# Kernel optimization log

Measured on AMD Instinct MI355X. Metric: run time of the kernel, lower is better.

## Reference

```python
import jax, jax.numpy as jnp
import numpy as np

B, N, C_IN = 32, 1024, 128
F0, F1, F2 = 64, 64, 64
OUT = 10
RATIOS = (0.8, 0.8)
EPS = 1e-5


def setup_inputs() -> dict:
    key = jax.random.key(0)
    ks = jax.random.split(key, 16)
    N_nodes = jax.random.randint(ks[0], (B,), N // 2, N + 1)
    mask = (jnp.arange(N)[None, :] < N_nodes[:, None]).astype(jnp.float32)
    x = jax.random.normal(ks[1], (B, N, C_IN), dtype=jnp.float32)
    # sparse-ish symmetric binary adjacency restricted to valid nodes
    A = (jax.random.uniform(ks[2], (B, N, N)) < 0.02).astype(jnp.float32)
    A = jnp.maximum(A, jnp.swapaxes(A, 1, 2))
    A = A * mask[:, :, None] * mask[:, None, :]
    def lin(k, fi, fo):
        b = 1.0 / np.sqrt(fi)
        kw, kb = jax.random.split(k)
        return (jax.random.uniform(kw, (fi, fo), minval=-b, maxval=b),
                jax.random.uniform(kb, (fo,), minval=-b, maxval=b))
    W0, b0 = lin(ks[3], C_IN, F0)
    W1, b1 = lin(ks[4], F0, F1)
    W2, b2 = lin(ks[5], F1, F2)
    bp0 = 1.0 / np.sqrt(F0)
    p0 = jax.random.uniform(ks[6], (F0, 1), minval=-bp0, maxval=bp0)
    bp1 = 1.0 / np.sqrt(F1)
    p1 = jax.random.uniform(ks[7], (F1, 1), minval=-bp1, maxval=bp1)
    Wfc, bfc = lin(ks[8], F2, OUT)
    return {"x": x, "A": A, "mask": mask, "N_nodes": N_nodes,
            "W0": W0, "b0": b0, "W1": W1, "b1": b1, "W2": W2, "b2": b2,
            "p0": p0, "p1": p1, "Wfc": Wfc, "bfc": bfc}


def _gconv(x, A, W, b):
    # Kipf-Welling normalized Laplacian conv, batched dense
    n = A.shape[1]
    A_hat = A + jnp.eye(n, dtype=A.dtype)[None]
    D = (jnp.sum(A_hat, axis=1) + EPS) ** -0.5  # [B,N]
    L = D[:, :, None] * A_hat * D[:, None, :]
    h = jnp.einsum('bnm,bmc->bnc', L, x) @ W + b
    return jax.nn.relu(h)


def _pool(x, A, mask, N_nodes, p, ratio):
    Bc, Nc, C = x.shape
    y = (x.reshape(Bc * Nc, C) @ p).reshape(Bc, Nc)
    y = y / jnp.sqrt(jnp.sum(p ** 2))
    N_remove = (N_nodes.astype(jnp.float32) * (1.0 - ratio)).astype(N_nodes.dtype)
    # remove the N_remove lowest-scoring valid nodes per graph
    y_eff = jnp.where(mask > 0, y, jnp.inf)
    ranks = jnp.argsort(jnp.argsort(y_eff, axis=1), axis=1)  # ascending rank
    new_mask = mask * (ranks >= N_remove[:, None]).astype(mask.dtype)
    x = x * jnp.tanh(y)[:, :, None] * new_mask[:, :, None]
    A = new_mask[:, :, None] * A * new_mask[:, None, :]
    return x, A, new_mask, N_nodes - N_remove


def reference(x, A, mask, N_nodes, W0, b0, W1, b1, W2, b2, p0, p1, Wfc, bfc):
    x = _gconv(x, A, W0, b0)
    x, A, mask, N_nodes = _pool(x, A, mask, N_nodes, p0, RATIOS[0])
    x = _gconv(x, A, W1, b1)
    x, A, mask, N_nodes = _pool(x, A, mask, N_nodes, p1, RATIOS[1])
    x = _gconv(x, A, W2, b2)
    x = jnp.max(x, axis=1)  # global max pool over nodes [B,F2]
    return x @ Wfc + bfc
```

## Files before the change

kernel.cpp:

```cpp
#include <hip/hip_runtime.h>
#include <cstdint>
#include <cstddef>

#define BB 32
#define NN 1024
#define CIN 128
#define FF 64
#define NOUT 10
#define CAP 128
#define EPSV 1e-5f

__global__ __launch_bounds__(256) void k_front(const float* __restrict__ A,
                                               const float* __restrict__ x,
                                               const float* __restrict__ W0,
                                               const int* __restrict__ Nn,
                                               const float* __restrict__ b2f,
                                               float* __restrict__ gmax,
                                               unsigned short* __restrict__ adj,
                                               int* __restrict__ cnt,
                                               float* __restrict__ c1,
                                               float* __restrict__ c2,
                                               float* __restrict__ T) {
    __shared__ __align__(16) float Wl[64 * 64];
    int tid = threadIdx.x;
    int wave = tid >> 6, lane = tid & 63;
    if (blockIdx.x >= 10240) {
        for (int i = tid; i < BB * 64; i += 256)
            gmax[i] = fmaxf(b2f[i & 63], 0.f);
        return;
    }
    if (blockIdx.x >= 8192) {
        int gid = blockIdx.x - 8192;
        int b = gid & 31;
        int cch = gid >> 5;
        if (cch * 16 >= Nn[b]) return;
        int row0 = (b << 10) + cch * 16;
        int rsub = lane >> 4, f0 = (lane & 15) * 4;
        int r = row0 + wave * 4 + rsub;
        const float4* xr = (const float4*)(x + (size_t)r * CIN);
        float4 acc = {0.f, 0.f, 0.f, 0.f};
#pragma unroll
        for (int kc = 0; kc < 2; ++kc) {
            if (kc) __syncthreads();
            for (int t = tid; t < 64 * 16; t += 256)
                ((float4*)Wl)[t] = ((const float4*)W0)[kc * 1024 + t];
            __syncthreads();
#pragma unroll 4
            for (int k4 = 0; k4 < 16; ++k4) {
                float4 xv = xr[kc * 16 + k4];
                float4 w0 = *(const float4*)&Wl[(k4 * 4 + 0) * 64 + f0];
                float4 w1 = *(const float4*)&Wl[(k4 * 4 + 1) * 64 + f0];
                float4 w2 = *(const float4*)&Wl[(k4 * 4 + 2) * 64 + f0];
                float4 w3 = *(const float4*)&Wl[(k4 * 4 + 3) * 64 + f0];
                acc.x += xv.x * w0.x; acc.y += xv.x * w0.y; acc.z += xv.x * w0.z; acc.w += xv.x * w0.w;
                acc.x += xv.y * w1.x; acc.y += xv.y * w1.y; acc.z += xv.y * w1.z; acc.w += xv.y * w1.w;
                acc.x += xv.z * w2.x; acc.y += xv.z * w2.y; acc.z += xv.z * w2.z; acc.w += xv.z * w2.w;
                acc.x += xv.w * w3.x; acc.y += xv.w * w3.y; acc.z += xv.w * w3.z; acc.w += xv.w * w3.w;
            }
        }
        *(float4*)&T[(size_t)r * 64 + f0] = acc;
    } else {
        int r = blockIdx.x * 4 + wave;
        int b = r >> 10;
        int Nb = Nn[b];
        int rl = r & 1023;
        if (rl >= Nb) {
            if (lane == 0) {
                cnt[r] = 0;
                float D = 1.0f / sqrtf(1.0f + EPSV);
                c1[r] = D;
                c2[r] = D * D;
            }
            return;
        }
        unsigned short* adjs = ((unsigned short*)Wl) + wave * CAP;
        const float4* Arow = (const float4*)(A + (size_t)r * NN);
        int nch = (Nb + 255) >> 8;
        float4 z4 = {0.f, 0.f, 0.f, 0.f};
        float4 v0 = Arow[lane];
        float4 v1 = Arow[64 + lane];
        float4 v2 = (nch > 2) ? Arow[128 + lane] : z4;
        float4 v3 = (nch > 3) ? Arow[192 + lane] : z4;
        int c = 0;
        unsigned long long lt = (lane == 0) ? 0ULL : ((1ULL << lane) - 1ULL);
        float4 vv[4] = {v0, v1, v2, v3};
#pragma unroll
        for (int it = 0; it < 4; ++it) {
            float4 v = vv[it];
            int j0 = it * 256 + lane * 4;
            unsigned long long m0 = __ballot(v.x != 0.f);
            unsigned long long m1 = __ballot(v.y != 0.f);
            unsigned long long m2 = __ballot(v.z != 0.f);
            unsigned long long m3 = __ballot(v.w != 0.f);
            int before = __popcll(m0 & lt) + __popcll(m1 & lt) +
                         __popcll(m2 & lt) + __popcll(m3 & lt);
            int p = c + before;
            if (v.x != 0.f) { if (p < CAP) adjs[p] = (unsigned short)(j0 + 0); ++p; }
            if (v.y != 0.f) { if (p < CAP) adjs[p] = (unsigned short)(j0 + 1); ++p; }
            if (v.z != 0.f) { if (p < CAP) adjs[p] = (unsigned short)(j0 + 2); ++p; }
            if (v.w != 0.f) { if (p < CAP) adjs[p] = (unsigned short)(j0 + 3); ++p; }
            c += __popcll(m0) + __popcll(m1) + __popcll(m2) + __popcll(m3);
        }
        int cc = (c > CAP) ? CAP : c;
        uint32_t* dst = (uint32_t*)(adj + (size_t)r * CAP);
        if (lane * 2 < cc) dst[lane] = ((const uint32_t*)adjs)[lane];
        if (lane == 0) {
            cnt[r] = cc;
            float D = 1.0f / sqrtf((float)c + 1.0f + EPSV);
            c1[r] = D;
            c2[r] = D * D;
        }
    }
}

__global__ __launch_bounds__(256) void k_spmm1(const unsigned short* __restrict__ adj,
                                               const int* __restrict__ cnt,
                                               const float* __restrict__ c1,
                                               const float* __restrict__ c2,
                                               const float* __restrict__ T,
                                               const float* __restrict__ bias,
                                               const float* __restrict__ p,
                                               float* __restrict__ y,
                                               const float* __restrict__ Wn,
                                               float* __restrict__ Tout,
                                               const int* __restrict__ Nn) {
    __shared__ __align__(16) float c1s[NN];
    int b   = blockIdx.x & 31;
    int cch = blockIdx.x >> 5;
    int Nb = Nn[b];
    if (cch * 16 >= Nb) return;
    int tid = threadIdx.x;
    int n4 = (Nb + 3) >> 2;
    if (tid < n4) ((float4*)c1s)[tid] = ((const float4*)(c1 + (b << 10)))[tid];
    __syncthreads();
    int wave = tid >> 6, lane = tid & 63;
    int r0 = (b << 10) + cch * 16 + wave * 4;
    const float* Tb = T + ((size_t)(b << 10) << 6);
    float bv = bias[lane];
    float pv = p[lane];
    float pp = pv * pv;
    for (int s = 32; s; s >>= 1) pp += __shfl_xor(pp, s, 64);
    float ppinv = 1.0f / sqrtf(pp);
#pragma unroll
    for (int rr = 0; rr < 4; ++rr) {
        int r = r0 + rr;
        int rl = r & 1023;
        if (rl >= Nb) break;
        const unsigned short* arow = adj + (size_t)r * CAP;
        int n = cnt[r];
        float acc0 = 0.f, acc1 = 0.f, acc2 = 0.f, acc3 = 0.f;
        int t = 0;
        for (; t + 4 <= n; t += 4) {
            ushort4 j4 = *(const ushort4*)(arow + t);
            acc0 += c1s[j4.x] * Tb[((int)j4.x << 6) + lane];
            acc1 += c1s[j4.y] * Tb[((int)j4.y << 6) + lane];
            acc2 += c1s[j4.z] * Tb[((int)j4.z << 6) + lane];
            acc3 += c1s[j4.w] * Tb[((int)j4.w << 6) + lane];
        }
        for (; t < n; ++t) {
            int j = arow[t];
            acc0 += c1s[j] * Tb[(j << 6) + lane];
        }
        float acc = (acc0 + acc1) + (acc2 + acc3);
        float o = c1s[rl] * acc + c2[r] * T[((size_t)r << 6) + lane] + bv;
        o = fmaxf(o, 0.f);
        {
            float a = o * pv;
            for (int s = 32; s; s >>= 1) a += __shfl_xor(a, s, 64);
            if (lane == 0) y[r] = a * ppinv;
        }
        {
            float tac = 0.f;
#pragma unroll 16
            for (int k = 0; k < 64; ++k)
                tac = fmaf(__shfl(o, k, 64), Wn[(k << 6) + lane], tac);
            Tout[((size_t)r << 6) + lane] = tac;
        }
    }
}

__global__ __launch_bounds__(256) void k_rankdeg(const float* __restrict__ y,
                                                 const float* __restrict__ maskSrc,
                                                 const int* __restrict__ nsrc,
                                                 const int* __restrict__ Nn,
                                                 const unsigned short* __restrict__ adj,
                                                 const int* __restrict__ cnt,
                                                 float* __restrict__ nmOut,
                                                 int* __restrict__ ncur,
                                                 float* __restrict__ csrcO,
                                                 float* __restrict__ scsO) {
    __shared__ __align__(16) float yv[NN];
    __shared__ __align__(16) unsigned long long kv[NN];
    __shared__ float nml[NN];
    int b = blockIdx.x;
    int tid = threadIdx.x;
    const float INF = __builtin_inff();
    int Nb = Nn[b];
    {
        float4 v;
        if (tid * 4 < Nb) {
            v = ((const float4*)(y + (b << 10)))[tid];
            float4 m = ((const float4*)(maskSrc + (b << 10)))[tid];
            v.x = (m.x > 0.f) ? v.x : INF;
            v.y = (m.y > 0.f) ? v.y : INF;
            v.z = (m.z > 0.f) ? v.z : INF;
            v.w = (m.w > 0.f) ? v.w : INF;
        } else {
            v.x = INF; v.y = INF; v.z = INF; v.w = INF;
        }
        ((float4*)yv)[tid] = v;
    }
    int n = nsrc[b];
    const float RM = (float)(1.0 - 0.8);
    int nrem = (int)((float)n * RM);
    if (tid == 0) ncur[b] = n - nrem;
    __syncthreads();
#pragma unroll
    for (int t = 0; t < 4; ++t) {
        int i = tid + (t << 8);
        unsigned int u = __float_as_uint(yv[i]);
        u ^= (unsigned int)((int)u >> 31) | 0x80000000u;
        kv[i] = ((unsigned long long)u << 10) | (unsigned int)i;
    }
    __syncthreads();
    unsigned long long k0 = kv[tid], k1 = kv[tid + 256],
                       k2 = kv[tid + 512], k3 = kv[tid + 768];
    int r0 = 0, r1 = 0, r2 = 0, r3 = 0;
    int nkc = (Nb + 1) >> 1;
#pragma unroll 4
    for (int c = 0; c < nkc; ++c) {
        ulonglong2 a = ((const ulonglong2*)kv)[c];
        r0 += (a.x < k0) + (a.y < k0);
        r1 += (a.x < k1) + (a.y < k1);
        r2 += (a.x < k2) + (a.y < k2);
        r3 += (a.x < k3) + (a.y < k3);
    }
    int rk[4] = {r0, r1, r2, r3};
#pragma unroll
    for (int t = 0; t < 4; ++t) {
        int i = tid + (t << 8);
        float nmv = (yv[i] < INF && rk[t] >= nrem) ? 1.f : 0.f;
        nml[i] = nmv;
        nmOut[(b << 10) + i] = nmv;
    }
    __syncthreads();
#pragma unroll
    for (int t = 0; t < 4; ++t) {
        int i = tid + (t << 8);
        if (i < Nb) {
            int gr = (b << 10) + i;
            float m = nml[i];
            int nn = cnt[gr];
            const unsigned short* ar = adj + (size_t)gr * CAP;
            float s = 0.f;
            int tt = 0;
            for (; tt + 4 <= nn; tt += 4) {
                ushort4 j4 = *(const ushort4*)(ar + tt);
                s += nml[j4.x] + nml[j4.y] + nml[j4.z] + nml[j4.w];
            }
            for (; tt < nn; ++tt) s += nml[ar[tt]];
            float D = 1.0f / sqrtf(m * s + 1.0f + EPSV);
            csrcO[gr] = m * D;
            scsO[gr] = tanhf(yv[i]) * m;
        }
    }
}

__global__ __launch_bounds__(256) void k_spmm23(const unsigned short* __restrict__ adj,
                                                const int* __restrict__ cnt,
                                                const float* __restrict__ csrc,
                                                const float* __restrict__ scs,
                                                const float* __restrict__ Tin,
                                                const float* __restrict__ bias,
                                                const float* __restrict__ p,
                                                float* __restrict__ y,
                                                const float* __restrict__ Wn,
                                                float* __restrict__ Tout,
                                                float* __restrict__ gmax,
                                                const int* __restrict__ Nn) {
    __shared__ __align__(16) float csrcs[NN];
    __shared__ __align__(16) float scss[NN];
    __shared__ float red[4][64];
    int b   = blockIdx.x & 31;
    int cch = blockIdx.x >> 5;
    int Nb = Nn[b];
    if (cch * 16 >= Nb) return;
    int tid = threadIdx.x;
    int n4 = (Nb + 3) >> 2;
    if (tid < n4) {
        ((float4*)csrcs)[tid] = ((const float4*)(csrc + (b << 10)))[tid];
        ((float4*)scss)[tid]  = ((const float4*)(scs  + (b << 10)))[tid];
    }
    __syncthreads();
    int wave = tid >> 6, lane = tid & 63;
    int r0 = (b << 10) + cch * 16 + wave * 4;
    const float* Tb = Tin + ((size_t)(b << 10) << 6);
    float bv = bias[lane];
    float pv = 0.f, ppinv = 0.f;
    if (p != nullptr) {
        pv = p[lane];
        float pp = pv * pv;
        for (int s = 32; s; s >>= 1) pp += __shfl_xor(pp, s, 64);
        ppinv = 1.0f / sqrtf(pp);
    }
    float vmax = 0.f;
#pragma unroll
    for (int rr = 0; rr < 4; ++rr) {
        int r = r0 + rr;
        int rl = r & 1023;
        if (rl >= Nb) break;
        const unsigned short* arow = adj + (size_t)r * CAP;
        int n = cnt[r];
        float acc0 = 0.f, acc1 = 0.f, acc2 = 0.f, acc3 = 0.f;
        int t = 0;
        for (; t + 4 <= n; t += 4) {
            ushort4 j4 = *(const ushort4*)(arow + t);
            acc0 += csrcs[j4.x] * (scss[j4.x] * Tb[((int)j4.x << 6) + lane]);
            acc1 += csrcs[j4.y] * (scss[j4.y] * Tb[((int)j4.y << 6) + lane]);
            acc2 += csrcs[j4.z] * (scss[j4.z] * Tb[((int)j4.z << 6) + lane]);
            acc3 += csrcs[j4.w] * (scss[j4.w] * Tb[((int)j4.w << 6) + lane]);
        }
        for (; t < n; ++t) {
            int j = arow[t];
            acc0 += csrcs[j] * (scss[j] * Tb[(j << 6) + lane]);
        }
        float acc = (acc0 + acc1) + (acc2 + acc3);
        float cd = csrcs[rl];
        float selfv = scss[rl] * Tin[((size_t)r << 6) + lane];
        float o = cd * acc + (cd * cd) * selfv + bv;
        o = fmaxf(o, 0.f);
        if (p != nullptr) {
            float a = o * pv;
            for (int s = 32; s; s >>= 1) a += __shfl_xor(a, s, 64);
            if (lane == 0) y[r] = a * ppinv;
        }
        if (Wn != nullptr) {
            float tac = 0.f;
#pragma unroll 16
            for (int k = 0; k < 64; ++k)
                tac = fmaf(__shfl(o, k, 64), Wn[(k << 6) + lane], tac);
            Tout[((size_t)r << 6) + lane] = tac;
        }
        vmax = fmaxf(vmax, o);
    }
    if (gmax != nullptr) {
        red[wave][lane] = vmax;
        __syncthreads();
        if (wave == 0) {
            float m = fmaxf(fmaxf(red[0][lane], red[1][lane]),
                            fmaxf(red[2][lane], red[3][lane]));
            atomicMax((int*)&gmax[(b << 6) + lane], __float_as_int(m));
        }
    }
}

__global__ __launch_bounds__(64) void k_fc(const float* __restrict__ gmax,
                                           const float* __restrict__ Wfc,
                                           const float* __restrict__ bfc,
                                           float* __restrict__ out) {
    __shared__ float gl[64];
    int b = blockIdx.x, lane = threadIdx.x;
    gl[lane] = gmax[(b << 6) + lane];
    __syncthreads();
    if (lane < NOUT) {
        float acc = bfc[lane];
        for (int k = 0; k < 64; ++k) acc += gl[k] * Wfc[k * NOUT + lane];
        out[b * NOUT + lane] = acc;
    }
}

extern "C" void kernel_launch(void* const* d_in, const int* in_sizes, int n_in,
                              void* d_out, int out_size, void* d_ws, size_t ws_size,
                              hipStream_t stream) {
    const float* x    = (const float*)d_in[0];
    const float* A    = (const float*)d_in[1];
    const float* mask = (const float*)d_in[2];
    const int*   Nn   = (const int*)d_in[3];
    const float* W0   = (const float*)d_in[4];
    const float* b0   = (const float*)d_in[5];
    const float* W1   = (const float*)d_in[6];
    const float* b1   = (const float*)d_in[7];
    const float* W2   = (const float*)d_in[8];
    const float* b2   = (const float*)d_in[9];
    const float* p0   = (const float*)d_in[10];
    const float* p1   = (const float*)d_in[11];
    const float* Wfc  = (const float*)d_in[12];
    const float* bfc  = (const float*)d_in[13];
    float* out = (float*)d_out;

    char* ws = (char*)d_ws;
    size_t off = 0;
    auto alloc = [&](size_t bytes) -> void* {
        void* p = ws + off;
        off = (off + bytes + 255) & ~(size_t)255;
        return p;
    };
    unsigned short* adj = (unsigned short*)alloc((size_t)BB * NN * CAP * 2);
    int*   cnt  = (int*)  alloc((size_t)BB * NN * 4);
    float* X    = (float*)alloc((size_t)BB * NN * 64 * 4);
    float* T    = (float*)alloc((size_t)BB * NN * 64 * 4);
    float* c1   = (float*)alloc((size_t)BB * NN * 4);
    float* c2   = (float*)alloc((size_t)BB * NN * 4);
    float* y    = (float*)alloc((size_t)BB * NN * 4);
    float* nm0  = (float*)alloc((size_t)BB * NN * 4);
    float* nm1  = (float*)alloc((size_t)BB * NN * 4);
    int*   nc0  = (int*)  alloc((size_t)BB * 4);
    int*   nc1  = (int*)  alloc((size_t)BB * 4);
    float* gmax = (float*)alloc((size_t)BB * 64 * 4);

    k_front<<<8192 + 2048 + 1, 256, 0, stream>>>(A, x, W0, Nn, b2, gmax,
                                                 adj, cnt, c1, c2, T);
    k_spmm1<<<2048, 256, 0, stream>>>(adj, cnt, c1, c2, T, b0, p0, y, W1, X, Nn);
    k_rankdeg<<<BB, 256, 0, stream>>>(y, mask, Nn, Nn, adj, cnt, nm0, nc0, c1, c2);
    k_spmm23<<<2048, 256, 0, stream>>>(adj, cnt, c1, c2, X, b1, p1, y, W2, T,
                                       nullptr, Nn);
    k_rankdeg<<<BB, 256, 0, stream>>>(y, nm0, nc0, Nn, adj, cnt, nm1, nc1, c1, c2);
    k_spmm23<<<2048, 256, 0, stream>>>(adj, cnt, c1, c2, T, b2, nullptr, nullptr,
                                       nullptr, nullptr, gmax, Nn);
    k_fc<<<BB, 64, 0, stream>>>(gmax, Wfc, bfc, out);
}
```

Before: 409.4 us.

## Aggregate-then-transform in sparse convs, split rank kernel, nontemporal input loads

The layer-2 and layer-3 graph convs now aggregate neighbours first, then apply the weight matrix through an LDS-staged 4-wide matmul, replacing the per-row shuffle-based transform. Rows removed by pooling are skipped. The rank/degree kernel is spread over 16 blocks per graph and uses a wave-parallel neighbour-mask sum, which raises parallelism beyond 32 blocks. Each sub-block still recomputes the full sort, so that work is duplicated. The large one-shot reads of A and x use nontemporal loads to reduce cache pollution.

```diff
diff --git a/kernel.cpp b/kernel.cpp
--- a/kernel.cpp
+++ b/kernel.cpp
@@ -9,6 +9,12 @@
 #define NOUT 10
 #define CAP 128
 #define EPSV 1e-5f
+
+typedef float vf4 __attribute__((ext_vector_type(4)));
+__device__ __forceinline__ float4 ldnt(const float4* p) {
+    vf4 v = __builtin_nontemporal_load((const vf4*)p);
+    return make_float4(v.x, v.y, v.z, v.w);
+}
 
 __global__ __launch_bounds__(256) void k_front(const float* __restrict__ A,
                                                const float* __restrict__ x,
@@ -47,7 +53,7 @@
             __syncthreads();
 #pragma unroll 4
             for (int k4 = 0; k4 < 16; ++k4) {
-                float4 xv = xr[kc * 16 + k4];
+                float4 xv = ldnt(xr + kc * 16 + k4);
                 float4 w0 = *(const float4*)&Wl[(k4 * 4 + 0) * 64 + f0];
                 float4 w1 = *(const float4*)&Wl[(k4 * 4 + 1) * 64 + f0];
                 float4 w2 = *(const float4*)&Wl[(k4 * 4 + 2) * 64 + f0];
@@ -77,10 +83,10 @@
         const float4* Arow = (const float4*)(A + (size_t)r * NN);
         int nch = (Nb + 255) >> 8;
         float4 z4 = {0.f, 0.f, 0.f, 0.f};
-        float4 v0 = Arow[lane];
-        float4 v1 = Arow[64 + lane];
-        float4 v2 = (nch > 2) ? Arow[128 + lane] : z4;
-        float4 v3 = (nch > 3) ? Arow[192 + lane] : z4;
+        float4 v0 = ldnt(Arow + lane);
+        float4 v1 = ldnt(Arow + 64 + lane);
+        float4 v2 = (nch > 2) ? ldnt(Arow + 128 + lane) : z4;
+        float4 v3 = (nch > 3) ? ldnt(Arow + 192 + lane) : z4;
         int c = 0;
         unsigned long long lt = (lane == 0) ? 0ULL : ((1ULL << lane) - 1ULL);
         float4 vv[4] = {v0, v1, v2, v3};
@@ -113,17 +119,16 @@
     }
 }
 
-__global__ __launch_bounds__(256) void k_spmm1(const unsigned short* __restrict__ adj,
-                                               const int* __restrict__ cnt,
-                                               const float* __restrict__ c1,
-                                               const float* __restrict__ c2,
-                                               const float* __restrict__ T,
-                                               const float* __restrict__ bias,
-                                               const float* __restrict__ p,
-                                               float* __restrict__ y,
-                                               const float* __restrict__ Wn,
-                                               float* __restrict__ Tout,
-                                               const int* __restrict__ Nn) {
+__global__ __launch_bounds__(256) void k_spmm(const unsigned short* __restrict__ adj,
+                                              const int* __restrict__ cnt,
+                                              const float* __restrict__ c1,
+                                              const float* __restrict__ c2,
+                                              const float* __restrict__ T,
+                                              const float* __restrict__ bias,
+                                              float* __restrict__ X,
+                                              const float* __restrict__ p,
+                                              float* __restrict__ y,
+                                              const int* __restrict__ Nn) {
     __shared__ __align__(16) float c1s[NN];
     int b   = blockIdx.x & 31;
     int cch = blockIdx.x >> 5;
@@ -164,18 +169,10 @@
         float acc = (acc0 + acc1) + (acc2 + acc3);
         float o = c1s[rl] * acc + c2[r] * T[((size_t)r << 6) + lane] + bv;
         o = fmaxf(o, 0.f);
-        {
-            float a = o * pv;
-            for (int s = 32; s; s >>= 1) a += __shfl_xor(a, s, 64);
-            if (lane == 0) y[r] = a * ppinv;
-        }
-        {
-            float tac = 0.f;
-#pragma unroll 16
-            for (int k = 0; k < 64; ++k)
-                tac = fmaf(__shfl(o, k, 64), Wn[(k << 6) + lane], tac);
-            Tout[((size_t)r << 6) + lane] = tac;
-        }
+        X[((size_t)r << 6) + lane] = o;
+        float a = o * pv;
+        for (int s = 32; s; s >>= 1) a += __shfl_xor(a, s, 64);
+        if (lane == 0) y[r] = a * ppinv;
     }
 }
 
@@ -187,15 +184,18 @@
                                                  const int* __restrict__ cnt,
                                                  float* __restrict__ nmOut,
                                                  int* __restrict__ ncur,
-                                                 float* __restrict__ csrcO,
-                                                 float* __restrict__ scsO) {
+                                                 float* __restrict__ cg,
+                                                 float* __restrict__ c1o,
+                                                 float* __restrict__ cso) {
     __shared__ __align__(16) float yv[NN];
     __shared__ __align__(16) unsigned long long kv[NN];
     __shared__ float nml[NN];
-    int b = blockIdx.x;
+    int b = blockIdx.x >> 4;
+    int sub = blockIdx.x & 15;
     int tid = threadIdx.x;
     const float INF = __builtin_inff();
     int Nb = Nn[b];
+    if ((sub << 6) >= Nb) return;
     {
         float4 v;
         if (tid * 4 < Nb) {
@@ -213,7 +213,7 @@
     int n = nsrc[b];
     const float RM = (float)(1.0 - 0.8);
     int nrem = (int)((float)n * RM);
-    if (tid == 0) ncur[b] = n - nrem;
+    if (sub == 0 && tid == 0) ncur[b] = n - nrem;
     __syncthreads();
 #pragma unroll
     for (int t = 0; t < 4; ++t) {
@@ -239,117 +239,147 @@
 #pragma unroll
     for (int t = 0; t < 4; ++t) {
         int i = tid + (t << 8);
-        float nmv = (yv[i] < INF && rk[t] >= nrem) ? 1.f : 0.f;
-        nml[i] = nmv;
-        nmOut[(b << 10) + i] = nmv;
-    }
-    __syncthreads();
-#pragma unroll
-    for (int t = 0; t < 4; ++t) {
-        int i = tid + (t << 8);
-        if (i < Nb) {
-            int gr = (b << 10) + i;
-            float m = nml[i];
+        nml[i] = (yv[i] < INF && rk[t] >= nrem) ? 1.f : 0.f;
+    }
+    __syncthreads();
+    int wave = tid >> 6, lane = tid & 63;
+    for (int rd = 0; rd < 16; ++rd) {
+        int i = (sub << 6) + (rd << 2) + wave;
+        int gr = (b << 10) + i;
+        if (i >= Nb) {
+            if (lane == 0) nmOut[gr] = 0.f;
+            continue;
+        }
+        float m = nml[i];
+        float s = 0.f;
+        if (m != 0.f) {
             int nn = cnt[gr];
             const unsigned short* ar = adj + (size_t)gr * CAP;
-            float s = 0.f;
-            int tt = 0;
-            for (; tt + 4 <= nn; tt += 4) {
-                ushort4 j4 = *(const ushort4*)(ar + tt);
-                s += nml[j4.x] + nml[j4.y] + nml[j4.z] + nml[j4.w];
-            }
-            for (; tt < nn; ++tt) s += nml[ar[tt]];
+            if (lane < nn)      s  = nml[ar[lane]];
+            if (lane + 64 < nn) s += nml[ar[lane + 64]];
+            for (int sh = 32; sh; sh >>= 1) s += __shfl_xor(s, sh, 64);
+        }
+        if (lane == 0) {
+            nmOut[gr] = m;
             float D = 1.0f / sqrtf(m * s + 1.0f + EPSV);
-            csrcO[gr] = m * D;
-            scsO[gr] = tanhf(yv[i]) * m;
-        }
-    }
-}
-
-__global__ __launch_bounds__(256) void k_spmm23(const unsigned short* __restrict__ adj,
-                                                const int* __restrict__ cnt,
-                                                const float* __restrict__ csrc,
-                                                const float* __restrict__ scs,
-                                                const float* __restrict__ Tin,
-                                                const float* __restrict__ bias,
-                                                const float* __restrict__ p,
-                                                float* __restrict__ y,
-                                                const float* __restrict__ Wn,
-                                                float* __restrict__ Tout,
-                                                float* __restrict__ gmax,
-                                                const int* __restrict__ Nn) {
-    __shared__ __align__(16) float csrcs[NN];
-    __shared__ __align__(16) float scss[NN];
-    __shared__ float red[4][64];
+            float th = tanhf(yv[i]);
+            cg[gr]  = (m * D) * th;
+            c1o[gr] = m * D;
+            cso[gr] = m * (D * D) * th;
+        }
+    }
+}
+
+__global__ __launch_bounds__(256) void k_spmmW(const unsigned short* __restrict__ adj,
+                                               const int* __restrict__ cnt,
+                                               const float* __restrict__ cg,
+                                               const float* __restrict__ c1,
+                                               const float* __restrict__ cs,
+                                               const float* __restrict__ Xin,
+                                               const float* __restrict__ W,
+                                               const float* __restrict__ bias,
+                                               const float* __restrict__ p,
+                                               float* __restrict__ y,
+                                               float* __restrict__ Xout,
+                                               float* __restrict__ gmax,
+                                               const int* __restrict__ Nn) {
+    __shared__ __align__(16) float Wl[64 * 64];
+    __shared__ __align__(16) float cgs[NN];
+    __shared__ __align__(16) float aggl[4][4][68];
+    __shared__ float4 red4[4][16];
     int b   = blockIdx.x & 31;
     int cch = blockIdx.x >> 5;
     int Nb = Nn[b];
     if (cch * 16 >= Nb) return;
     int tid = threadIdx.x;
+    for (int t = tid; t < 64 * 16; t += 256)
+        ((float4*)Wl)[t] = ((const float4*)W)[t];
     int n4 = (Nb + 3) >> 2;
-    if (tid < n4) {
-        ((float4*)csrcs)[tid] = ((const float4*)(csrc + (b << 10)))[tid];
-        ((float4*)scss)[tid]  = ((const float4*)(scs  + (b << 10)))[tid];
-    }
+    if (tid < n4) ((float4*)cgs)[tid] = ((const float4*)(cg + (b << 10)))[tid];
     __syncthreads();
     int wave = tid >> 6, lane = tid & 63;
     int r0 = (b << 10) + cch * 16 + wave * 4;
-    const float* Tb = Tin + ((size_t)(b << 10) << 6);
-    float bv = bias[lane];
-    float pv = 0.f, ppinv = 0.f;
-    if (p != nullptr) {
-        pv = p[lane];
-        float pp = pv * pv;
-        for (int s = 32; s; s >>= 1) pp += __shfl_xor(pp, s, 64);
-        ppinv = 1.0f / sqrtf(pp);
-    }
-    float vmax = 0.f;
+    const float* Xb = Xin + ((size_t)(b << 10) << 6);
+    int umask = 0;
 #pragma unroll
     for (int rr = 0; rr < 4; ++rr) {
         int r = r0 + rr;
         int rl = r & 1023;
-        if (rl >= Nb) break;
-        const unsigned short* arow = adj + (size_t)r * CAP;
-        int n = cnt[r];
-        float acc0 = 0.f, acc1 = 0.f, acc2 = 0.f, acc3 = 0.f;
-        int t = 0;
-        for (; t + 4 <= n; t += 4) {
-            ushort4 j4 = *(const ushort4*)(arow + t);
-            acc0 += csrcs[j4.x] * (scss[j4.x] * Tb[((int)j4.x << 6) + lane]);
-            acc1 += csrcs[j4.y] * (scss[j4.y] * Tb[((int)j4.y << 6) + lane]);
-            acc2 += csrcs[j4.z] * (scss[j4.z] * Tb[((int)j4.z << 6) + lane]);
-            acc3 += csrcs[j4.w] * (scss[j4.w] * Tb[((int)j4.w << 6) + lane]);
-        }
-        for (; t < n; ++t) {
-            int j = arow[t];
-            acc0 += csrcs[j] * (scss[j] * Tb[(j << 6) + lane]);
-        }
-        float acc = (acc0 + acc1) + (acc2 + acc3);
-        float cd = csrcs[rl];
-        float selfv = scss[rl] * Tin[((size_t)r << 6) + lane];
-        float o = cd * acc + (cd * cd) * selfv + bv;
-        o = fmaxf(o, 0.f);
-        if (p != nullptr) {
-            float a = o * pv;
-            for (int s = 32; s; s >>= 1) a += __shfl_xor(a, s, 64);
-            if (lane == 0) y[r] = a * ppinv;
-        }
-        if (Wn != nullptr) {
-            float tac = 0.f;
+        float aggv = 0.f;
+        if (rl < Nb) {
+            float c1r = c1[r];
+            if (c1r != 0.f) {
+                umask |= 1 << rr;
+                const unsigned short* arow = adj + (size_t)r * CAP;
+                int n = cnt[r];
+                float acc0 = 0.f, acc1 = 0.f, acc2 = 0.f, acc3 = 0.f;
+                int t = 0;
+                for (; t + 4 <= n; t += 4) {
+                    ushort4 j4 = *(const ushort4*)(arow + t);
+                    acc0 += cgs[j4.x] * Xb[((int)j4.x << 6) + lane];
+                    acc1 += cgs[j4.y] * Xb[((int)j4.y << 6) + lane];
+                    acc2 += cgs[j4.z] * Xb[((int)j4.z << 6) + lane];
+                    acc3 += cgs[j4.w] * Xb[((int)j4.w << 6) + lane];
+                }
+                for (; t < n; ++t) {
+                    int j = arow[t];
+                    acc0 += cgs[j] * Xb[(j << 6) + lane];
+                }
+                float acc = (acc0 + acc1) + (acc2 + acc3);
+                aggv = c1r * acc + cs[r] * Xin[((size_t)r << 6) + lane];
+            }
+        }
+        aggl[wave][rr][lane] = aggv;
+    }
+    int rsub = lane >> 4, f0 = (lane & 15) * 4;
+    float4 o4 = *(const float4*)&bias[f0];
 #pragma unroll 16
-            for (int k = 0; k < 64; ++k)
-                tac = fmaf(__shfl(o, k, 64), Wn[(k << 6) + lane], tac);
-            Tout[((size_t)r << 6) + lane] = tac;
-        }
-        vmax = fmaxf(vmax, o);
+    for (int k = 0; k < 64; ++k) {
+        float a = aggl[wave][rsub][k];
+        float4 w = *(const float4*)&Wl[(k << 6) + f0];
+        o4.x = fmaf(a, w.x, o4.x); o4.y = fmaf(a, w.y, o4.y);
+        o4.z = fmaf(a, w.z, o4.z); o4.w = fmaf(a, w.w, o4.w);
+    }
+    o4.x = fmaxf(o4.x, 0.f); o4.y = fmaxf(o4.y, 0.f);
+    o4.z = fmaxf(o4.z, 0.f); o4.w = fmaxf(o4.w, 0.f);
+    bool live = (umask >> rsub) & 1;
+    int rOut = r0 + rsub;
+    if (Xout != nullptr && live)
+        *(float4*)&Xout[((size_t)rOut << 6) + f0] = o4;
+    if (p != nullptr) {
+        float4 p4 = *(const float4*)&p[f0];
+        float pp = p4.x * p4.x + p4.y * p4.y + p4.z * p4.z + p4.w * p4.w;
+        for (int s = 8; s; s >>= 1) pp += __shfl_xor(pp, s, 64);
+        float ppinv = 1.0f / sqrtf(pp);
+        float a = o4.x * p4.x + o4.y * p4.y + o4.z * p4.z + o4.w * p4.w;
+        for (int s = 8; s; s >>= 1) a += __shfl_xor(a, s, 64);
+        if ((lane & 15) == 0 && live) y[rOut] = a * ppinv;
     }
     if (gmax != nullptr) {
-        red[wave][lane] = vmax;
+        float4 m4 = o4;
+        m4.x = fmaxf(m4.x, __shfl_xor(m4.x, 16, 64));
+        m4.y = fmaxf(m4.y, __shfl_xor(m4.y, 16, 64));
+        m4.z = fmaxf(m4.z, __shfl_xor(m4.z, 16, 64));
+        m4.w = fmaxf(m4.w, __shfl_xor(m4.w, 16, 64));
+        m4.x = fmaxf(m4.x, __shfl_xor(m4.x, 32, 64));
+        m4.y = fmaxf(m4.y, __shfl_xor(m4.y, 32, 64));
+        m4.z = fmaxf(m4.z, __shfl_xor(m4.z, 32, 64));
+        m4.w = fmaxf(m4.w, __shfl_xor(m4.w, 32, 64));
+        if (lane < 16) red4[wave][lane] = m4;
         __syncthreads();
-        if (wave == 0) {
-            float m = fmaxf(fmaxf(red[0][lane], red[1][lane]),
-                            fmaxf(red[2][lane], red[3][lane]));
-            atomicMax((int*)&gmax[(b << 6) + lane], __float_as_int(m));
+        if (wave == 0 && lane < 16) {
+            float4 a0 = red4[0][lane], a1 = red4[1][lane];
+            float4 a2 = red4[2][lane], a3 = red4[3][lane];
+            float4 mm;
+            mm.x = fmaxf(fmaxf(a0.x, a1.x), fmaxf(a2.x, a3.x));
+            mm.y = fmaxf(fmaxf(a0.y, a1.y), fmaxf(a2.y, a3.y));
+            mm.z = fmaxf(fmaxf(a0.z, a1.z), fmaxf(a2.z, a3.z));
+            mm.w = fmaxf(fmaxf(a0.w, a1.w), fmaxf(a2.w, a3.w));
+            int base = (b << 6) + lane * 4;
+            atomicMax((int*)&gmax[base + 0], __float_as_int(mm.x));
+            atomicMax((int*)&gmax[base + 1], __float_as_int(mm.y));
+            atomicMax((int*)&gmax[base + 2], __float_as_int(mm.z));
+            atomicMax((int*)&gmax[base + 3], __float_as_int(mm.w));
         }
     }
 }
@@ -401,6 +431,7 @@
     float* T    = (float*)alloc((size_t)BB * NN * 64 * 4);
     float* c1   = (float*)alloc((size_t)BB * NN * 4);
     float* c2   = (float*)alloc((size_t)BB * NN * 4);
+    float* cg   = (float*)alloc((size_t)BB * NN * 4);
     float* y    = (float*)alloc((size_t)BB * NN * 4);
     float* nm0  = (float*)alloc((size_t)BB * NN * 4);
     float* nm1  = (float*)alloc((size_t)BB * NN * 4);
@@ -410,12 +441,14 @@
 
     k_front<<<8192 + 2048 + 1, 256, 0, stream>>>(A, x, W0, Nn, b2, gmax,
                                                  adj, cnt, c1, c2, T);
-    k_spmm1<<<2048, 256, 0, stream>>>(adj, cnt, c1, c2, T, b0, p0, y, W1, X, Nn);
-    k_rankdeg<<<BB, 256, 0, stream>>>(y, mask, Nn, Nn, adj, cnt, nm0, nc0, c1, c2);
-    k_spmm23<<<2048, 256, 0, stream>>>(adj, cnt, c1, c2, X, b1, p1, y, W2, T,
-                                       nullptr, Nn);
-    k_rankdeg<<<BB, 256, 0, stream>>>(y, nm0, nc0, Nn, adj, cnt, nm1, nc1, c1, c2);
-    k_spmm23<<<2048, 256, 0, stream>>>(adj, cnt, c1, c2, T, b2, nullptr, nullptr,
-                                       nullptr, nullptr, gmax, Nn);
+    k_spmm<<<2048, 256, 0, stream>>>(adj, cnt, c1, c2, T, b0, X, p0, y, Nn);
+    k_rankdeg<<<BB * 16, 256, 0, stream>>>(y, mask, Nn, Nn, adj, cnt,
+                                           nm0, nc0, cg, c1, c2);
+    k_spmmW<<<2048, 256, 0, stream>>>(adj, cnt, cg, c1, c2, X, W1, b1,
+                                      p1, y, T, nullptr, Nn);
+    k_rankdeg<<<BB * 16, 256, 0, stream>>>(y, nm0, nc0, Nn, adj, cnt,
+                                           nm1, nc1, cg, c1, c2);
+    k_spmmW<<<2048, 256, 0, stream>>>(adj, cnt, cg, c1, c2, T, W2, b2,
+                                      nullptr, nullptr, nullptr, gmax, Nn);
     k_fc<<<BB, 64, 0, stream>>>(gmax, Wfc, bfc, out);
 }
```

Result: no change. 416.8 us (+1.8%).
